# Optimization experiments

Hardware: AMD Instinct MI355X
Metric: run time of the kernel (lower is better)

Reference implementation:

```python
import jax, jax.numpy as jnp
import numpy as np
import math

N_ROWS, N_COLS, N_DEPTHS = 4, 4, 2
N_BLOCKS = N_ROWS * N_COLS * N_DEPTHS
N_BASIS = 50
BAND_LOW, BAND_HIGH = 1.0, 20.0
N_POINTS = 131072


def _build_spectral_kernel(n_basis, band_low, band_high, seed):
    rng = np.random.default_rng(seed)
    def _s1d(n):
        u = rng.uniform(0, 1, n)
        half = band_high - band_low
        val = u * 2 * half
        return np.where(val < half, val - band_high, val - half + band_low)
    ky, kx, kz = _s1d(n_basis), _s1d(n_basis), _s1d(n_basis)
    return np.stack((ky, kx, kz), axis=0).astype(np.float32)  # [3, M]


def setup_inputs() -> dict:
    key = jax.random.key(0)
    k1, k2 = jax.random.split(key)
    coords = jax.random.uniform(k1, (N_POINTS, 3), dtype=jnp.float32)
    K = _build_spectral_kernel(N_BASIS, BAND_LOW, BAND_HIGH, seed=0)  # [3, M]
    kernels = jnp.broadcast_to(jnp.asarray(K)[None], (N_BLOCKS, 3, N_BASIS)).copy()
    # weights are zeros at init in the module; use small random values so the
    # forward output is non-trivial for correctness testing.
    weights = 0.1 * jax.random.normal(k2, (N_BLOCKS, N_BASIS), dtype=jnp.float32)
    bias = jnp.full((N_BLOCKS,), math.log(0.3 / 0.7), dtype=jnp.float32)
    return {"coords": coords, "kernels": kernels, "weights": weights, "bias": bias}


def _block_indices(coords):
    ys, xs, zs = coords[:, 0], coords[:, 1], coords[:, 2]
    my, My = ys.min(), ys.max()
    mx, Mx = xs.min(), xs.max()
    mz, Mz = zs.min(), zs.max()
    row = jnp.clip(((ys - my) / (My - my + 1e-9) * N_ROWS).astype(jnp.int32), 0, N_ROWS - 1)
    col = jnp.clip(((xs - mx) / (Mx - mx + 1e-9) * N_COLS).astype(jnp.int32), 0, N_COLS - 1)
    dep = jnp.clip(((zs - mz) / (Mz - mz + 1e-9) * N_DEPTHS).astype(jnp.int32), 0, N_DEPTHS - 1)
    return row * (N_COLS * N_DEPTHS) + col * N_DEPTHS + dep  # [N]


def reference(coords, kernels, weights, bias):
    N = coords.shape[0]
    B, _, M = kernels.shape
    K_flat = jnp.transpose(kernels, (1, 0, 2)).reshape(3, B * M)  # [3, B*M]
    z = (coords @ K_flat).reshape(N, B, M) + 1.0                   # [N, B, M]
    out_all = jax.nn.sigmoid(jnp.einsum('nbm,bm->nb', jnp.sin(z), weights) + bias[None, :])
    bidx = _block_indices(coords)                                  # [N] int
    # hard gather: one block per point (overlap <= 0 branch)
    return jnp.take_along_axis(out_all, bidx[:, None], axis=1)     # [N, 1]
```

## Files before the change

kernel.cpp:

```cpp
#include <hip/hip_runtime.h>
#include <math.h>

#define NROWS   4
#define NCOLS   4
#define NDEPTHS 2
#define NBLK    32
#define NBASIS  50
#define REDB    128

__global__ __launch_bounds__(256) void minmax_partial(
    const float4* __restrict__ coords4, int nunits, float* __restrict__ part)
{
    float mn0 =  INFINITY, mn1 =  INFINITY, mn2 =  INFINITY;
    float mx0 = -INFINITY, mx1 = -INFINITY, mx2 = -INFINITY;
    int stride = gridDim.x * blockDim.x;
    for (int u = blockIdx.x * blockDim.x + threadIdx.x; u < nunits; u += stride) {
        float4 a = coords4[3*u+0];
        float4 b = coords4[3*u+1];
        float4 c = coords4[3*u+2];
        mn0 = fminf(mn0, fminf(fminf(a.x, a.w), fminf(b.z, c.y)));
        mx0 = fmaxf(mx0, fmaxf(fmaxf(a.x, a.w), fmaxf(b.z, c.y)));
        mn1 = fminf(mn1, fminf(fminf(a.y, b.x), fminf(b.w, c.z)));
        mx1 = fmaxf(mx1, fmaxf(fmaxf(a.y, b.x), fmaxf(b.w, c.z)));
        mn2 = fminf(mn2, fminf(fminf(a.z, b.y), fminf(c.x, c.w)));
        mx2 = fmaxf(mx2, fmaxf(fmaxf(a.z, b.y), fmaxf(c.x, c.w)));
    }
    #pragma unroll
    for (int off = 32; off; off >>= 1) {
        mn0 = fminf(mn0, __shfl_xor(mn0, off));
        mn1 = fminf(mn1, __shfl_xor(mn1, off));
        mn2 = fminf(mn2, __shfl_xor(mn2, off));
        mx0 = fmaxf(mx0, __shfl_xor(mx0, off));
        mx1 = fmaxf(mx1, __shfl_xor(mx1, off));
        mx2 = fmaxf(mx2, __shfl_xor(mx2, off));
    }
    __shared__ float sm[4][6];
    int wave = threadIdx.x >> 6;
    int lane = threadIdx.x & 63;
    if (lane == 0) {
        sm[wave][0] = mn0; sm[wave][1] = mn1; sm[wave][2] = mn2;
        sm[wave][3] = mx0; sm[wave][4] = mx1; sm[wave][5] = mx2;
    }
    __syncthreads();
    if (threadIdx.x == 0) {
        float r0 = sm[0][0], r1 = sm[0][1], r2 = sm[0][2];
        float r3 = sm[0][3], r4 = sm[0][4], r5 = sm[0][5];
        #pragma unroll
        for (int w = 1; w < 4; ++w) {
            r0 = fminf(r0, sm[w][0]); r1 = fminf(r1, sm[w][1]); r2 = fminf(r2, sm[w][2]);
            r3 = fmaxf(r3, sm[w][3]); r4 = fmaxf(r4, sm[w][4]); r5 = fmaxf(r5, sm[w][5]);
        }
        part[0*REDB + blockIdx.x] = r0;
        part[1*REDB + blockIdx.x] = r1;
        part[2*REDB + blockIdx.x] = r2;
        part[3*REDB + blockIdx.x] = r3;
        part[4*REDB + blockIdx.x] = r4;
        part[5*REDB + blockIdx.x] = r5;
    }
}

__global__ __launch_bounds__(256) void blocknet(
    const float* __restrict__ coords,
    const float* __restrict__ kernels,
    const float* __restrict__ weights,
    const float* __restrict__ bias,
    const float* __restrict__ part,
    float* __restrict__ out, int n)
{
    __shared__ float wT[NBASIS][NBLK];
    __shared__ float bS[NBLK];
    __shared__ float cross[4][6];
    __shared__ float fin[6];

    int t = threadIdx.x;

    for (int i = t; i < NBLK * NBASIS; i += 256) {
        int m = i >> 5;
        int b = i & 31;
        wT[m][b] = weights[b * NBASIS + m];
    }
    if (t < NBLK) bS[t] = bias[t];

    float v0, v1, v2, v3, v4, v5;
    if (t < REDB) {
        v0 = part[0*REDB + t]; v1 = part[1*REDB + t]; v2 = part[2*REDB + t];
        v3 = part[3*REDB + t]; v4 = part[4*REDB + t]; v5 = part[5*REDB + t];
    } else {
        v0 = v1 = v2 = INFINITY; v3 = v4 = v5 = -INFINITY;
    }
    #pragma unroll
    for (int off = 32; off; off >>= 1) {
        v0 = fminf(v0, __shfl_xor(v0, off));
        v1 = fminf(v1, __shfl_xor(v1, off));
        v2 = fminf(v2, __shfl_xor(v2, off));
        v3 = fmaxf(v3, __shfl_xor(v3, off));
        v4 = fmaxf(v4, __shfl_xor(v4, off));
        v5 = fmaxf(v5, __shfl_xor(v5, off));
    }
    int wave = t >> 6, lane = t & 63;
    if (lane == 0) {
        cross[wave][0] = v0; cross[wave][1] = v1; cross[wave][2] = v2;
        cross[wave][3] = v3; cross[wave][4] = v4; cross[wave][5] = v5;
    }
    __syncthreads();
    if (t == 0) {
        float r0 = fminf(cross[0][0], cross[1][0]);
        float r1 = fminf(cross[0][1], cross[1][1]);
        float r2 = fminf(cross[0][2], cross[1][2]);
        float r3 = fmaxf(cross[0][3], cross[1][3]);
        float r4 = fmaxf(cross[0][4], cross[1][4]);
        float r5 = fmaxf(cross[0][5], cross[1][5]);
        fin[0] = r0; fin[1] = r1; fin[2] = r2;
        fin[3] = (r3 - r0) + 1e-9f;
        fin[4] = (r4 - r1) + 1e-9f;
        fin[5] = (r5 - r2) + 1e-9f;
    }
    __syncthreads();

    int i = blockIdx.x * 256 + t;
    if (i >= n) return;

    float y  = coords[3*i+0];
    float x  = coords[3*i+1];
    float zc = coords[3*i+2];

    int row = (int)((y  - fin[0]) / fin[3] * (float)NROWS);
    int col = (int)((x  - fin[1]) / fin[4] * (float)NCOLS);
    int dep = (int)((zc - fin[2]) / fin[5] * (float)NDEPTHS);
    row = min(max(row, 0), NROWS - 1);
    col = min(max(col, 0), NCOLS - 1);
    dep = min(max(dep, 0), NDEPTHS - 1);
    int b = row * (NCOLS * NDEPTHS) + col * NDEPTHS + dep;

    const float* __restrict__ Ky = kernels;
    const float* __restrict__ Kx = kernels + NBASIS;
    const float* __restrict__ Kz = kernels + 2*NBASIS;

    float acc = 0.0f;
    #pragma unroll
    for (int m = 0; m < NBASIS; ++m) {
        float zz = fmaf(y, Ky[m], fmaf(x, Kx[m], fmaf(zc, Kz[m], 1.0f)));
        acc = fmaf(__sinf(zz), wT[m][b], acc);
    }
    float s = acc + bS[b];
    out[i] = __builtin_amdgcn_rcpf(1.0f + __expf(-s));
}

extern "C" void kernel_launch(void* const* d_in, const int* in_sizes, int n_in,
                              void* d_out, int out_size, void* d_ws, size_t ws_size,
                              hipStream_t stream)
{
    const float* coords  = (const float*)d_in[0];
    const float* kernels = (const float*)d_in[1];
    const float* weights = (const float*)d_in[2];
    const float* bias    = (const float*)d_in[3];
    float* part = (float*)d_ws;
    int n = in_sizes[0] / 3;

    int nunits = (in_sizes[0] + 11) / 12;
    hipLaunchKernelGGL(minmax_partial, dim3(REDB), dim3(256), 0, stream,
                       (const float4*)coords, nunits, part);
    int nb = (n + 255) / 256;
    hipLaunchKernelGGL(blocknet, dim3(nb), dim3(256), 0, stream,
                       coords, kernels, weights, bias, part, (float*)d_out, n);
}
```

Baseline: 14.87 us.

## Fuse min/max reduction and evaluation into one cooperative kernel with grid sync

Merges the separate partial min/max kernel and the evaluation kernel into a single cooperative launch. Each block reduces the coordinates it already loaded, writes per-block partials, then waits at a grid-wide barrier. After the barrier every block reduces all partials and evaluates its points using the coordinates held in registers. This removes one kernel launch and a second read of the coordinates. In exchange it adds a grid-wide barrier, has every block reread all the partials, and relies on all 512 blocks being co-resident.

```diff
diff --git a/kernel.cpp b/kernel.cpp
--- a/kernel.cpp
+++ b/kernel.cpp
@@ -1,30 +1,45 @@
 #include <hip/hip_runtime.h>
+#include <hip/hip_cooperative_groups.h>
 #include <math.h>
+
+namespace cg = cooperative_groups;
 
 #define NROWS   4
 #define NCOLS   4
 #define NDEPTHS 2
 #define NBLK    32
 #define NBASIS  50
-#define REDB    128
 
-__global__ __launch_bounds__(256) void minmax_partial(
-    const float4* __restrict__ coords4, int nunits, float* __restrict__ part)
+__global__ __launch_bounds__(256) void fused_blocknet(
+    const float* __restrict__ coords,
+    const float* __restrict__ kernels,
+    const float* __restrict__ weights,
+    const float* __restrict__ bias,
+    float* __restrict__ part,
+    float* __restrict__ out, int n)
 {
-    float mn0 =  INFINITY, mn1 =  INFINITY, mn2 =  INFINITY;
-    float mx0 = -INFINITY, mx1 = -INFINITY, mx2 = -INFINITY;
-    int stride = gridDim.x * blockDim.x;
-    for (int u = blockIdx.x * blockDim.x + threadIdx.x; u < nunits; u += stride) {
-        float4 a = coords4[3*u+0];
-        float4 b = coords4[3*u+1];
-        float4 c = coords4[3*u+2];
-        mn0 = fminf(mn0, fminf(fminf(a.x, a.w), fminf(b.z, c.y)));
-        mx0 = fmaxf(mx0, fmaxf(fmaxf(a.x, a.w), fmaxf(b.z, c.y)));
-        mn1 = fminf(mn1, fminf(fminf(a.y, b.x), fminf(b.w, c.z)));
-        mx1 = fmaxf(mx1, fmaxf(fmaxf(a.y, b.x), fmaxf(b.w, c.z)));
-        mn2 = fminf(mn2, fminf(fminf(a.z, b.y), fminf(c.x, c.w)));
-        mx2 = fmaxf(mx2, fmaxf(fmaxf(a.z, b.y), fmaxf(c.x, c.w)));
+    __shared__ float wT[NBASIS][NBLK];
+    __shared__ float bS[NBLK];
+    __shared__ float cross[4][6];
+    __shared__ float fin[6];
+
+    const int t    = threadIdx.x;
+    const int nb   = gridDim.x;
+    const int blk  = blockIdx.x;
+    const int gi   = blk * 256 + t;
+    const int i    = gi < n ? gi : n - 1;
+
+    for (int idx = t; idx < NBLK * NBASIS; idx += 256) {
+        int m = idx >> 5, b = idx & 31;
+        wT[m][b] = weights[b * NBASIS + m];
     }
+    if (t < NBLK) bS[t] = bias[t];
+
+    float y  = coords[3*i+0];
+    float x  = coords[3*i+1];
+    float zc = coords[3*i+2];
+
+    float mn0=y, mx0=y, mn1=x, mx1=x, mn2=zc, mx2=zc;
     #pragma unroll
     for (int off = 32; off; off >>= 1) {
         mn0 = fminf(mn0, __shfl_xor(mn0, off));
@@ -34,59 +49,31 @@
         mx1 = fmaxf(mx1, __shfl_xor(mx1, off));
         mx2 = fmaxf(mx2, __shfl_xor(mx2, off));
     }
-    __shared__ float sm[4][6];
-    int wave = threadIdx.x >> 6;
-    int lane = threadIdx.x & 63;
+    const int wave = t >> 6, lane = t & 63;
     if (lane == 0) {
-        sm[wave][0] = mn0; sm[wave][1] = mn1; sm[wave][2] = mn2;
-        sm[wave][3] = mx0; sm[wave][4] = mx1; sm[wave][5] = mx2;
+        cross[wave][0]=mn0; cross[wave][1]=mn1; cross[wave][2]=mn2;
+        cross[wave][3]=mx0; cross[wave][4]=mx1; cross[wave][5]=mx2;
     }
     __syncthreads();
-    if (threadIdx.x == 0) {
-        float r0 = sm[0][0], r1 = sm[0][1], r2 = sm[0][2];
-        float r3 = sm[0][3], r4 = sm[0][4], r5 = sm[0][5];
+    if (t == 0) {
+        float r0=cross[0][0], r1=cross[0][1], r2=cross[0][2];
+        float r3=cross[0][3], r4=cross[0][4], r5=cross[0][5];
         #pragma unroll
         for (int w = 1; w < 4; ++w) {
-            r0 = fminf(r0, sm[w][0]); r1 = fminf(r1, sm[w][1]); r2 = fminf(r2, sm[w][2]);
-            r3 = fmaxf(r3, sm[w][3]); r4 = fmaxf(r4, sm[w][4]); r5 = fmaxf(r5, sm[w][5]);
+            r0=fminf(r0,cross[w][0]); r1=fminf(r1,cross[w][1]); r2=fminf(r2,cross[w][2]);
+            r3=fmaxf(r3,cross[w][3]); r4=fmaxf(r4,cross[w][4]); r5=fmaxf(r5,cross[w][5]);
         }
-        part[0*REDB + blockIdx.x] = r0;
-        part[1*REDB + blockIdx.x] = r1;
-        part[2*REDB + blockIdx.x] = r2;
-        part[3*REDB + blockIdx.x] = r3;
-        part[4*REDB + blockIdx.x] = r4;
-        part[5*REDB + blockIdx.x] = r5;
+        part[0*nb+blk]=r0; part[1*nb+blk]=r1; part[2*nb+blk]=r2;
+        part[3*nb+blk]=r3; part[4*nb+blk]=r4; part[5*nb+blk]=r5;
     }
-}
 
-__global__ __launch_bounds__(256) void blocknet(
-    const float* __restrict__ coords,
-    const float* __restrict__ kernels,
-    const float* __restrict__ weights,
-    const float* __restrict__ bias,
-    const float* __restrict__ part,
-    float* __restrict__ out, int n)
-{
-    __shared__ float wT[NBASIS][NBLK];
-    __shared__ float bS[NBLK];
-    __shared__ float cross[4][6];
-    __shared__ float fin[6];
+    cg::this_grid().sync();
 
-    int t = threadIdx.x;
-
-    for (int i = t; i < NBLK * NBASIS; i += 256) {
-        int m = i >> 5;
-        int b = i & 31;
-        wT[m][b] = weights[b * NBASIS + m];
-    }
-    if (t < NBLK) bS[t] = bias[t];
-
-    float v0, v1, v2, v3, v4, v5;
-    if (t < REDB) {
-        v0 = part[0*REDB + t]; v1 = part[1*REDB + t]; v2 = part[2*REDB + t];
-        v3 = part[3*REDB + t]; v4 = part[4*REDB + t]; v5 = part[5*REDB + t];
-    } else {
-        v0 = v1 = v2 = INFINITY; v3 = v4 = v5 = -INFINITY;
+    float v0=INFINITY, v1=INFINITY, v2=INFINITY;
+    float v3=-INFINITY, v4=-INFINITY, v5=-INFINITY;
+    for (int e = t; e < nb; e += 256) {
+        v0=fminf(v0, part[0*nb+e]); v1=fminf(v1, part[1*nb+e]); v2=fminf(v2, part[2*nb+e]);
+        v3=fmaxf(v3, part[3*nb+e]); v4=fmaxf(v4, part[4*nb+e]); v5=fmaxf(v5, part[5*nb+e]);
     }
     #pragma unroll
     for (int off = 32; off; off >>= 1) {
@@ -97,32 +84,27 @@
         v4 = fmaxf(v4, __shfl_xor(v4, off));
         v5 = fmaxf(v5, __shfl_xor(v5, off));
     }
-    int wave = t >> 6, lane = t & 63;
     if (lane == 0) {
-        cross[wave][0] = v0; cross[wave][1] = v1; cross[wave][2] = v2;
-        cross[wave][3] = v3; cross[wave][4] = v4; cross[wave][5] = v5;
+        cross[wave][0]=v0; cross[wave][1]=v1; cross[wave][2]=v2;
+        cross[wave][3]=v3; cross[wave][4]=v4; cross[wave][5]=v5;
     }
     __syncthreads();
     if (t == 0) {
-        float r0 = fminf(cross[0][0], cross[1][0]);
-        float r1 = fminf(cross[0][1], cross[1][1]);
-        float r2 = fminf(cross[0][2], cross[1][2]);
-        float r3 = fmaxf(cross[0][3], cross[1][3]);
-        float r4 = fmaxf(cross[0][4], cross[1][4]);
-        float r5 = fmaxf(cross[0][5], cross[1][5]);
-        fin[0] = r0; fin[1] = r1; fin[2] = r2;
-        fin[3] = (r3 - r0) + 1e-9f;
-        fin[4] = (r4 - r1) + 1e-9f;
-        fin[5] = (r5 - r2) + 1e-9f;
+        float r0=cross[0][0], r1=cross[0][1], r2=cross[0][2];
+        float r3=cross[0][3], r4=cross[0][4], r5=cross[0][5];
+        #pragma unroll
+        for (int w = 1; w < 4; ++w) {
+            r0=fminf(r0,cross[w][0]); r1=fminf(r1,cross[w][1]); r2=fminf(r2,cross[w][2]);
+            r3=fmaxf(r3,cross[w][3]); r4=fmaxf(r4,cross[w][4]); r5=fmaxf(r5,cross[w][5]);
+        }
+        fin[0]=r0; fin[1]=r1; fin[2]=r2;
+        fin[3]=(r3-r0)+1e-9f;
+        fin[4]=(r4-r1)+1e-9f;
+        fin[5]=(r5-r2)+1e-9f;
     }
     __syncthreads();
 
-    int i = blockIdx.x * 256 + t;
-    if (i >= n) return;
-
-    float y  = coords[3*i+0];
-    float x  = coords[3*i+1];
-    float zc = coords[3*i+2];
+    if (gi >= n) return;
 
     int row = (int)((y  - fin[0]) / fin[3] * (float)NROWS);
     int col = (int)((x  - fin[1]) / fin[4] * (float)NCOLS);
@@ -143,7 +125,7 @@
         acc = fmaf(__sinf(zz), wT[m][b], acc);
     }
     float s = acc + bS[b];
-    out[i] = __builtin_amdgcn_rcpf(1.0f + __expf(-s));
+    out[gi] = __builtin_amdgcn_rcpf(1.0f + __expf(-s));
 }
 
 extern "C" void kernel_launch(void* const* d_in, const int* in_sizes, int n_in,
@@ -155,12 +137,12 @@
     const float* weights = (const float*)d_in[2];
     const float* bias    = (const float*)d_in[3];
     float* part = (float*)d_ws;
-    int n = in_sizes[0] / 3;
+    float* outp = (float*)d_out;
+    int n  = in_sizes[0] / 3;
+    int nb = (n + 255) / 256;
 
-    int nunits = (in_sizes[0] + 11) / 12;
-    hipLaunchKernelGGL(minmax_partial, dim3(REDB), dim3(256), 0, stream,
-                       (const float4*)coords, nunits, part);
-    int nb = (n + 255) / 256;
-    hipLaunchKernelGGL(blocknet, dim3(nb), dim3(256), 0, stream,
-                       coords, kernels, weights, bias, part, (float*)d_out, n);
+    void* args[] = { (void*)&coords, (void*)&kernels, (void*)&weights,
+                     (void*)&bias, (void*)&part, (void*)&outp, (void*)&n };
+    hipLaunchCooperativeKernel((const void*)fused_blocknet, dim3(nb), dim3(256),
+                               args, 0, stream);
 }
```

After: 57.16 us. 3.84x slower.
